# Kernel optimization log

Measured on AMD Instinct MI355X. Metric: run time of the kernel, lower is better.

## Reference

```python
import jax, jax.numpy as jnp
import numpy as np

N = 6144        # total nodes
N_USER = 4096   # main nodes used by fusion head
R = 2           # nb_node_kinds (relations)
K = 3           # attention heads
F_IN = 25       # n_units[0]
F_OUT = 64      # n_units[1]
D2 = 64
NB_CLASSES = 2


def setup_inputs() -> dict:
    key = jax.random.key(0)
    ks = jax.random.split(key, 12)
    # boolean dense adjacency per relation, with guaranteed self-loops so no
    # softmax row is all -inf
    adj = jax.random.uniform(ks[0], (R, N, N)) < 0.01
    eye = jnp.eye(N, dtype=bool)
    hadj = adj | eye[None]
    h = jax.random.normal(ks[1], (N, F_IN), dtype=jnp.float32)
    s = 0.1
    return {
        "hadj": hadj,
        "h": h,
        # per-relation GAT params (xavier-ish scale)
        "w": jax.random.normal(ks[2], (R, K, F_IN, F_OUT), dtype=jnp.float32) * s,
        "a_src": jax.random.normal(ks[3], (R, K, F_OUT, 1), dtype=jnp.float32) * s,
        "a_dst": jax.random.normal(ks[4], (R, K, F_OUT, 1), dtype=jnp.float32) * s,
        "bias": jnp.zeros((R, F_OUT), dtype=jnp.float32),
        # additive attention (store Linear weights as (in, out))
        "aw1": jax.random.normal(ks[5], (F_IN, D2), dtype=jnp.float32) * s,
        "aw2": jax.random.normal(ks[6], (F_OUT, D2), dtype=jnp.float32) * s,
        "am": jax.random.normal(ks[7], (D2, 1), dtype=jnp.float32) * s,
        # fusion fc: in = F_OUT * (R + 1)
        "fc_w": jax.random.normal(ks[8], (F_OUT * (R + 1), NB_CLASSES), dtype=jnp.float32) * s,
        "fc_b": jnp.zeros((NB_CLASSES,), dtype=jnp.float32),
    }


def _gat(x, adj, W, asrc, adst, b):
    # x: (N, f_in), adj: (N, N) bool, W: (K, f_in, f_out)
    hp = jnp.einsum('nf,kfo->kno', x, W)                 # (K, N, f_out)
    s = jnp.einsum('kno,koj->kn', hp, asrc)              # (K, N)
    d = jnp.einsum('kno,koj->kn', hp, adst)              # (K, N)
    attn = s[:, :, None] + d[:, None, :]                 # (K, N, N)
    attn = jax.nn.leaky_relu(attn, negative_slope=0.2)
    attn = jnp.where(adj[None], attn, -jnp.inf)
    attn = jax.nn.softmax(attn, axis=-1)                 # dropout = identity (eval)
    out = jnp.einsum('knm,kmo->kno', attn, hp) + b[None, None, :]
    return out.mean(axis=0)                              # mean over heads -> (N, f_out)


def reference(hadj, h, w, a_src, a_dst, bias, aw1, aw2, am, fc_w, fc_b):
    # per-relation dense GAT (single layer; final layer -> mean over heads)
    embs = [_gat(h, hadj[r], w[r], a_src[r], a_dst[r], bias[r]) for r in range(R)]
    type_aware = jnp.stack([e[:N_USER] for e in embs], axis=1)   # (n_user, R, f_out)
    # additive attention fusion
    feat = h[:N_USER]                                            # (n_user, f_in)
    q = jnp.tanh(
        (feat @ aw1)[:, None, :] + jnp.einsum('nrf,fd->nrd', type_aware, aw2)
    )                                                            # (n_user, R, d2)
    beta = jax.nn.softmax(jnp.einsum('nrd,dj->nr', q, am), axis=-1)
    fusion = jnp.einsum('nr,nrf->nf', beta, type_aware)          # (n_user, f_out)
    cat = jnp.concatenate([type_aware.reshape(N_USER, -1), fusion], axis=-1)
    logits = cat @ fc_w + fc_b                                   # (n_user, nb_classes)
    return jax.nn.log_softmax(logits, axis=-1)
```

## Files before the change

kernel.cpp:

```cpp
#include <hip/hip_runtime.h>
#include <stdint.h>

#define NN 6144
#define NUSER 4096
#define RR 2
#define KK 3
#define FIN 25
#define FOUT 64
#define DD2 64
#define CAP 192

#define SCAN_BLOCKS (RR * NUSER / 4)
#define PROJ_BLOCKS (RR * NN / 4)

typedef int int4v __attribute__((ext_vector_type(4)));

__device__ __forceinline__ float wave_reduce_sum(float v) {
    #pragma unroll
    for (int off = 32; off >= 1; off >>= 1) v += __shfl_xor(v, off);
    return v;
}
__device__ __forceinline__ float wave_reduce_max(float v) {
    #pragma unroll
    for (int off = 32; off >= 1; off >>= 1) v = fmaxf(v, __shfl_xor(v, off));
    return v;
}
__device__ __forceinline__ unsigned short f2bf(float x) {
    unsigned int u = __float_as_uint(x);
    unsigned int r = (u + 0x7fffu + ((u >> 16) & 1u)) >> 16;
    return (unsigned short)r;
}
__device__ __forceinline__ float bf2f(unsigned short b) {
    return __uint_as_float(((unsigned int)b) << 16);
}

__global__ __launch_bounds__(256) void kAP_scan_proj(
    const int* __restrict__ hadj, int* __restrict__ cnt, int* __restrict__ idx,
    const float* __restrict__ h, const float* __restrict__ w,
    const float* __restrict__ asrc, const float* __restrict__ adst,
    ushort4* __restrict__ hpq, float4* __restrict__ sq, float4* __restrict__ dq)
{
    const int wid  = threadIdx.x >> 6;
    const int lane = threadIdx.x & 63;

    if (blockIdx.x < SCAN_BLOCKS) {
        const int urow = blockIdx.x * 4 + wid;
        const int r    = urow / NUSER;
        const int n    = urow - r * NUSER;
        const int* rowp   = hadj + ((size_t)r * NN + n) * NN;
        int*       rowidx = idx  + (size_t)urow * CAP;
        const unsigned long long below = (1ull << lane) - 1ull;

        int base = 0;
        #pragma unroll 8
        for (int t = 0; t < 24; ++t) {
            const int m0 = t * 256 + lane * 4;
            const int4v v = __builtin_nontemporal_load(
                reinterpret_cast<const int4v*>(rowp + m0));
            const unsigned long long b0 = __ballot(v.x != 0);
            const unsigned long long b1 = __ballot(v.y != 0);
            const unsigned long long b2 = __ballot(v.z != 0);
            const unsigned long long b3 = __ballot(v.w != 0);
            const int n0 = __popcll(b0), n1 = __popcll(b1);
            const int n2 = __popcll(b2), n3 = __popcll(b3);
            const int o0 = base + __popcll(b0 & below);
            const int o1 = base + n0 + __popcll(b1 & below);
            const int o2 = base + n0 + n1 + __popcll(b2 & below);
            const int o3 = base + n0 + n1 + n2 + __popcll(b3 & below);
            if (v.x && o0 < CAP) rowidx[o0] = m0 + 0;
            if (v.y && o1 < CAP) rowidx[o1] = m0 + 1;
            if (v.z && o2 < CAP) rowidx[o2] = m0 + 2;
            if (v.w && o3 < CAP) rowidx[o3] = m0 + 3;
            base += n0 + n1 + n2 + n3;
        }
        if (lane == 0) cnt[urow] = base > CAP ? CAP : base;
    } else {
        const int row = (blockIdx.x - SCAN_BLOCKS) * 4 + wid;
        const int r   = row / NN;
        const int n   = row % NN;

        const float* hrow = h + (size_t)n * FIN;
        float acc[KK];
        #pragma unroll
        for (int k = 0; k < KK; ++k) {
            const float* wp = w + ((size_t)(r * KK + k) * FIN) * FOUT + lane;
            float a = 0.f;
            #pragma unroll
            for (int f = 0; f < FIN; ++f) a += hrow[f] * wp[f * FOUT];
            acc[k] = a;
        }

        ushort4 pk;
        pk.x = f2bf(acc[0]); pk.y = f2bf(acc[1]); pk.z = f2bf(acc[2]); pk.w = 0;
        hpq[(size_t)row * FOUT + lane] = pk;

        float sv0 = wave_reduce_sum(acc[0] * asrc[(r * KK + 0) * FOUT + lane]);
        float sv1 = wave_reduce_sum(acc[1] * asrc[(r * KK + 1) * FOUT + lane]);
        float sv2 = wave_reduce_sum(acc[2] * asrc[(r * KK + 2) * FOUT + lane]);
        float dv0 = wave_reduce_sum(acc[0] * adst[(r * KK + 0) * FOUT + lane]);
        float dv1 = wave_reduce_sum(acc[1] * adst[(r * KK + 1) * FOUT + lane]);
        float dv2 = wave_reduce_sum(acc[2] * adst[(r * KK + 2) * FOUT + lane]);
        if (lane == 0) {
            sq[row] = make_float4(sv0, sv1, sv2, 0.f);
            dq[row] = make_float4(dv0, dv1, dv2, 0.f);
        }
    }
}

__global__ __launch_bounds__(256) void kB_gat(
    const int* __restrict__ cnt, const int* __restrict__ idx,
    const ushort4* __restrict__ hpq, const float4* __restrict__ sq,
    const float4* __restrict__ dq, const float* __restrict__ bias,
    float* __restrict__ embs)
{
    const int wid  = threadIdx.x >> 6;
    const int lane = threadIdx.x & 63;
    const int urow = blockIdx.x * 4 + wid;
    const int r    = urow / NUSER;
    const int n    = urow - r * NUSER;

    __shared__ int   nbr_s[4][CAP];
    __shared__ float pw_s[4][3][CAP];
    int* nbr = nbr_s[wid];
    float (*pw)[CAP] = pw_s[wid];

    const int count = cnt[urow];
    const int* rowidx = idx + (size_t)urow * CAP;

    const float4 sv = sq[(size_t)r * NN + n];
    const float4* dqr = dq + (size_t)r * NN;
    float mx0 = -1e30f, mx1 = -1e30f, mx2 = -1e30f;
    for (int j = lane; j < count; j += 64) {
        const int nb = rowidx[j];
        nbr[j] = nb;
        const float4 dv = dqr[nb];
        float e0 = sv.x + dv.x; e0 = (e0 >= 0.f) ? e0 : 0.2f * e0;
        float e1 = sv.y + dv.y; e1 = (e1 >= 0.f) ? e1 : 0.2f * e1;
        float e2 = sv.z + dv.z; e2 = (e2 >= 0.f) ? e2 : 0.2f * e2;
        pw[0][j] = e0; pw[1][j] = e1; pw[2][j] = e2;
        mx0 = fmaxf(mx0, e0); mx1 = fmaxf(mx1, e1); mx2 = fmaxf(mx2, e2);
    }
    mx0 = wave_reduce_max(mx0);
    mx1 = wave_reduce_max(mx1);
    mx2 = wave_reduce_max(mx2);

    float ss0 = 0.f, ss1 = 0.f, ss2 = 0.f;
    for (int j = lane; j < count; j += 64) {
        float p0 = __expf(pw[0][j] - mx0); pw[0][j] = p0; ss0 += p0;
        float p1 = __expf(pw[1][j] - mx1); pw[1][j] = p1; ss1 += p1;
        float p2 = __expf(pw[2][j] - mx2); pw[2][j] = p2; ss2 += p2;
    }
    ss0 = wave_reduce_sum(ss0);
    ss1 = wave_reduce_sum(ss1);
    ss2 = wave_reduce_sum(ss2);

    const ushort4* hq = hpq + ((size_t)r * NN) * FOUT + lane;
    float a0 = 0.f, a1 = 0.f, a2 = 0.f;
    int j = 0;
    for (; j + 4 <= count; j += 4) {
        #pragma unroll
        for (int u = 0; u < 4; ++u) {
            const ushort4 v = hq[(size_t)nbr[j + u] * FOUT];
            a0 += pw[0][j + u] * bf2f(v.x);
            a1 += pw[1][j + u] * bf2f(v.y);
            a2 += pw[2][j + u] * bf2f(v.z);
        }
    }
    for (; j < count; ++j) {
        const ushort4 v = hq[(size_t)nbr[j] * FOUT];
        a0 += pw[0][j] * bf2f(v.x);
        a1 += pw[1][j] * bf2f(v.y);
        a2 += pw[2][j] * bf2f(v.z);
    }

    const float tot = a0 / ss0 + a1 / ss1 + a2 / ss2;
    embs[(size_t)urow * FOUT + lane] = tot * (1.f / 3.f) + bias[r * FOUT + lane];
}

__global__ __launch_bounds__(64) void k3_fuse(
    const float* __restrict__ h, const float* __restrict__ embs,
    const float* __restrict__ aw1, const float* __restrict__ aw2,
    const float* __restrict__ am, const float* __restrict__ fcw,
    const float* __restrict__ fcb, float* __restrict__ out)
{
    const int n = blockIdx.x;
    const int o = threadIdx.x;

    __shared__ float sh[2][FOUT];
    const float ta0 = embs[((size_t)0 * NUSER + n) * FOUT + o];
    const float ta1 = embs[((size_t)1 * NUSER + n) * FOUT + o];
    sh[0][o] = ta0;
    sh[1][o] = ta1;

    float fa = 0.f;
    const float* hrow = h + (size_t)n * FIN;
    #pragma unroll
    for (int f = 0; f < FIN; ++f) fa += hrow[f] * aw1[f * DD2 + o];
    __syncthreads();

    float e[2];
    #pragma unroll
    for (int r = 0; r < 2; ++r) {
        float t = fa;
        #pragma unroll 8
        for (int j = 0; j < FOUT; ++j) t += sh[r][j] * aw2[j * DD2 + o];
        float q = tanhf(t);
        e[r] = wave_reduce_sum(q * am[o]);
    }
    const float mx = fmaxf(e[0], e[1]);
    float b0 = __expf(e[0] - mx), b1 = __expf(e[1] - mx);
    const float inv = 1.f / (b0 + b1);
    b0 *= inv; b1 *= inv;
    const float fus = b0 * ta0 + b1 * ta1;

    float p0 = ta0 * fcw[(o      ) * 2 + 0] + ta1 * fcw[(64 + o) * 2 + 0] + fus * fcw[(128 + o) * 2 + 0];
    float p1 = ta0 * fcw[(o      ) * 2 + 1] + ta1 * fcw[(64 + o) * 2 + 1] + fus * fcw[(128 + o) * 2 + 1];
    const float lg0 = wave_reduce_sum(p0) + fcb[0];
    const float lg1 = wave_reduce_sum(p1) + fcb[1];

    if (o == 0) {
        const float m2  = fmaxf(lg0, lg1);
        const float lse = m2 + logf(__expf(lg0 - m2) + __expf(lg1 - m2));
        out[(size_t)n * 2 + 0] = lg0 - lse;
        out[(size_t)n * 2 + 1] = lg1 - lse;
    }
}

extern "C" void kernel_launch(void* const* d_in, const int* in_sizes, int n_in,
                              void* d_out, int out_size, void* d_ws, size_t ws_size,
                              hipStream_t stream)
{
    const int*   hadj = (const int*)d_in[0];
    const float* h    = (const float*)d_in[1];
    const float* w    = (const float*)d_in[2];
    const float* asrc = (const float*)d_in[3];
    const float* adst = (const float*)d_in[4];
    const float* bias = (const float*)d_in[5];
    const float* aw1  = (const float*)d_in[6];
    const float* aw2  = (const float*)d_in[7];
    const float* am   = (const float*)d_in[8];
    const float* fcw  = (const float*)d_in[9];
    const float* fcb  = (const float*)d_in[10];
    float* out = (float*)d_out;

    char* ws = (char*)d_ws;
    ushort4* hpq = (ushort4*)ws;
    ws += (size_t)RR * NN * FOUT * sizeof(ushort4);
    float4* sq = (float4*)ws;
    ws += (size_t)RR * NN * sizeof(float4);
    float4* dq = (float4*)ws;
    ws += (size_t)RR * NN * sizeof(float4);
    float* embs = (float*)ws;
    ws += (size_t)RR * NUSER * FOUT * sizeof(float);
    int* cnt = (int*)ws;
    ws += (size_t)RR * NUSER * sizeof(int);
    int* idx = (int*)ws;

    kAP_scan_proj<<<SCAN_BLOCKS + PROJ_BLOCKS, 256, 0, stream>>>(
        hadj, cnt, idx, h, w, asrc, adst, hpq, sq, dq);
    kB_gat <<<RR * NUSER / 4, 256, 0, stream>>>(cnt, idx, hpq, sq, dq, bias, embs);
    k3_fuse<<<NUSER, 64, 0, stream>>>(h, embs, aw1, aw2, am, fcw, fcb, out);
}
```

Before: 86.68 us.

## Fuse GAT aggregation with fusion head and drop nontemporal scan loads

```diff
diff --git a/kernel.cpp b/kernel.cpp
--- a/kernel.cpp
+++ b/kernel.cpp
@@ -55,8 +55,7 @@
         #pragma unroll 8
         for (int t = 0; t < 24; ++t) {
             const int m0 = t * 256 + lane * 4;
-            const int4v v = __builtin_nontemporal_load(
-                reinterpret_cast<const int4v*>(rowp + m0));
+            const int4v v = *reinterpret_cast<const int4v*>(rowp + m0);
             const unsigned long long b0 = __ballot(v.x != 0);
             const unsigned long long b1 = __ballot(v.y != 0);
             const unsigned long long b2 = __ballot(v.z != 0);
@@ -107,22 +106,25 @@
     }
 }
 
-__global__ __launch_bounds__(256) void kB_gat(
+__global__ __launch_bounds__(128) void kBC_gat_fuse(
     const int* __restrict__ cnt, const int* __restrict__ idx,
     const ushort4* __restrict__ hpq, const float4* __restrict__ sq,
     const float4* __restrict__ dq, const float* __restrict__ bias,
-    float* __restrict__ embs)
+    const float* __restrict__ h, const float* __restrict__ aw1,
+    const float* __restrict__ aw2, const float* __restrict__ am,
+    const float* __restrict__ fcw, const float* __restrict__ fcb,
+    float* __restrict__ out)
 {
-    const int wid  = threadIdx.x >> 6;
+    const int n    = blockIdx.x;
+    const int r    = threadIdx.x >> 6;
     const int lane = threadIdx.x & 63;
-    const int urow = blockIdx.x * 4 + wid;
-    const int r    = urow / NUSER;
-    const int n    = urow - r * NUSER;
-
-    __shared__ int   nbr_s[4][CAP];
-    __shared__ float pw_s[4][3][CAP];
-    int* nbr = nbr_s[wid];
-    float (*pw)[CAP] = pw_s[wid];
+    const int urow = r * NUSER + n;
+
+    __shared__ int   nbr_s[2][CAP];
+    __shared__ float pw_s[2][3][CAP];
+    __shared__ float emb_s[2][FOUT];
+    int* nbr = nbr_s[r];
+    float (*pw)[CAP] = pw_s[r];
 
     const int count = cnt[urow];
     const int* rowidx = idx + (size_t)urow * CAP;
@@ -172,57 +174,46 @@
         a1 += pw[1][j] * bf2f(v.y);
         a2 += pw[2][j] * bf2f(v.z);
     }
-
-    const float tot = a0 / ss0 + a1 / ss1 + a2 / ss2;
-    embs[(size_t)urow * FOUT + lane] = tot * (1.f / 3.f) + bias[r * FOUT + lane];
-}
-
-__global__ __launch_bounds__(64) void k3_fuse(
-    const float* __restrict__ h, const float* __restrict__ embs,
-    const float* __restrict__ aw1, const float* __restrict__ aw2,
-    const float* __restrict__ am, const float* __restrict__ fcw,
-    const float* __restrict__ fcb, float* __restrict__ out)
-{
-    const int n = blockIdx.x;
-    const int o = threadIdx.x;
-
-    __shared__ float sh[2][FOUT];
-    const float ta0 = embs[((size_t)0 * NUSER + n) * FOUT + o];
-    const float ta1 = embs[((size_t)1 * NUSER + n) * FOUT + o];
-    sh[0][o] = ta0;
-    sh[1][o] = ta1;
-
-    float fa = 0.f;
-    const float* hrow = h + (size_t)n * FIN;
-    #pragma unroll
-    for (int f = 0; f < FIN; ++f) fa += hrow[f] * aw1[f * DD2 + o];
+    emb_s[r][lane] = (a0 / ss0 + a1 / ss1 + a2 / ss2) * (1.f / 3.f)
+                   + bias[r * FOUT + lane];
     __syncthreads();
 
-    float e[2];
-    #pragma unroll
-    for (int r = 0; r < 2; ++r) {
-        float t = fa;
-        #pragma unroll 8
-        for (int j = 0; j < FOUT; ++j) t += sh[r][j] * aw2[j * DD2 + o];
-        float q = tanhf(t);
-        e[r] = wave_reduce_sum(q * am[o]);
-    }
-    const float mx = fmaxf(e[0], e[1]);
-    float b0 = __expf(e[0] - mx), b1 = __expf(e[1] - mx);
-    const float inv = 1.f / (b0 + b1);
-    b0 *= inv; b1 *= inv;
-    const float fus = b0 * ta0 + b1 * ta1;
-
-    float p0 = ta0 * fcw[(o      ) * 2 + 0] + ta1 * fcw[(64 + o) * 2 + 0] + fus * fcw[(128 + o) * 2 + 0];
-    float p1 = ta0 * fcw[(o      ) * 2 + 1] + ta1 * fcw[(64 + o) * 2 + 1] + fus * fcw[(128 + o) * 2 + 1];
-    const float lg0 = wave_reduce_sum(p0) + fcb[0];
-    const float lg1 = wave_reduce_sum(p1) + fcb[1];
-
-    if (o == 0) {
-        const float m2  = fmaxf(lg0, lg1);
-        const float lse = m2 + logf(__expf(lg0 - m2) + __expf(lg1 - m2));
-        out[(size_t)n * 2 + 0] = lg0 - lse;
-        out[(size_t)n * 2 + 1] = lg1 - lse;
+    if (r == 0) {
+        const int o = lane;
+        const float ta0 = emb_s[0][o];
+        const float ta1 = emb_s[1][o];
+
+        float fa = 0.f;
+        const float* hrow = h + (size_t)n * FIN;
+        #pragma unroll
+        for (int f = 0; f < FIN; ++f) fa += hrow[f] * aw1[f * DD2 + o];
+
+        float e[2];
+        #pragma unroll
+        for (int rr = 0; rr < 2; ++rr) {
+            float t = fa;
+            #pragma unroll 8
+            for (int jj = 0; jj < FOUT; ++jj) t += emb_s[rr][jj] * aw2[jj * DD2 + o];
+            float q = tanhf(t);
+            e[rr] = wave_reduce_sum(q * am[o]);
+        }
+        const float mxe = fmaxf(e[0], e[1]);
+        float b0 = __expf(e[0] - mxe), b1 = __expf(e[1] - mxe);
+        const float inv = 1.f / (b0 + b1);
+        b0 *= inv; b1 *= inv;
+        const float fus = b0 * ta0 + b1 * ta1;
+
+        float p0 = ta0 * fcw[(o      ) * 2 + 0] + ta1 * fcw[(64 + o) * 2 + 0] + fus * fcw[(128 + o) * 2 + 0];
+        float p1 = ta0 * fcw[(o      ) * 2 + 1] + ta1 * fcw[(64 + o) * 2 + 1] + fus * fcw[(128 + o) * 2 + 1];
+        const float lg0 = wave_reduce_sum(p0) + fcb[0];
+        const float lg1 = wave_reduce_sum(p1) + fcb[1];
+
+        if (o == 0) {
+            const float m2  = fmaxf(lg0, lg1);
+            const float lse = m2 + logf(__expf(lg0 - m2) + __expf(lg1 - m2));
+            out[(size_t)n * 2 + 0] = lg0 - lse;
+            out[(size_t)n * 2 + 1] = lg1 - lse;
+        }
     }
 }
 
@@ -250,14 +241,12 @@
     ws += (size_t)RR * NN * sizeof(float4);
     float4* dq = (float4*)ws;
     ws += (size_t)RR * NN * sizeof(float4);
-    float* embs = (float*)ws;
-    ws += (size_t)RR * NUSER * FOUT * sizeof(float);
     int* cnt = (int*)ws;
     ws += (size_t)RR * NUSER * sizeof(int);
     int* idx = (int*)ws;
 
     kAP_scan_proj<<<SCAN_BLOCKS + PROJ_BLOCKS, 256, 0, stream>>>(
         hadj, cnt, idx, h, w, asrc, adst, hpq, sq, dq);
-    kB_gat <<<RR * NUSER / 4, 256, 0, stream>>>(cnt, idx, hpq, sq, dq, bias, embs);
-    k3_fuse<<<NUSER, 64, 0, stream>>>(h, embs, aw1, aw2, am, fcw, fcb, out);
-}
+    kBC_gat_fuse<<<NUSER, 128, 0, stream>>>(
+        cnt, idx, hpq, sq, dq, bias, h, aw1, aw2, am, fcw, fcb, out);
+}
```

After: 78.00 us, median of 2. 1.11x faster.
